# Kernel tuning notes

Hardware: AMD Instinct MI355X
Metric: run time of the kernel (lower is better)

The kernel has to match this reference:

```python
import jax, jax.numpy as jnp
import numpy as np

D_MODEL = 1024
N_HEADS = 16
D_EXP = 4
B, SQ, SKV = 2, 2048, 2048
LN_EPS = 1e-5


def _linear_params(key, d_in, d_out):
    kw, kb = jax.random.split(key)
    w = jax.random.normal(kw, (d_in, d_out), jnp.float32) * 0.02  # stored [in,out]
    b = jax.random.normal(kb, (d_out,), jnp.float32) * 0.02
    return w, b


def setup_inputs() -> dict:
    key = jax.random.key(0)
    ks = jax.random.split(key, 16)
    inp = {}
    inp["x"] = jax.random.normal(ks[0], (B, SQ, D_MODEL), jnp.float32)
    inp["encoder_out"] = jax.random.normal(ks[1], (B, SKV, D_MODEL), jnp.float32)
    # causal target mask, broadcast over batch and heads
    inp["tgt_mask"] = jnp.tril(jnp.ones((SQ, SQ), jnp.int32))[None, None]
    inp["src_mask"] = jnp.ones((1, 1, SQ, SKV), jnp.int32)
    # self-attention params
    inp["wq_s"], inp["bq_s"] = _linear_params(ks[2], D_MODEL, D_MODEL)
    inp["wk_s"], inp["bk_s"] = _linear_params(ks[3], D_MODEL, D_MODEL)
    inp["wv_s"], inp["bv_s"] = _linear_params(ks[4], D_MODEL, D_MODEL)
    inp["wo_s"], inp["bo_s"] = _linear_params(ks[5], D_MODEL, D_MODEL)
    # cross-attention params
    inp["wq_c"], inp["bq_c"] = _linear_params(ks[6], D_MODEL, D_MODEL)
    inp["wk_c"], inp["bk_c"] = _linear_params(ks[7], D_MODEL, D_MODEL)
    inp["wv_c"], inp["bv_c"] = _linear_params(ks[8], D_MODEL, D_MODEL)
    inp["wo_c"], inp["bo_c"] = _linear_params(ks[9], D_MODEL, D_MODEL)
    # feedforward params
    inp["ff1_w"], inp["ff1_b"] = _linear_params(ks[10], D_MODEL, D_MODEL * D_EXP)
    inp["ff2_w"], inp["ff2_b"] = _linear_params(ks[11], D_MODEL * D_EXP, D_MODEL)
    # layernorm params (3 AddNorms)
    for i, k in zip((1, 2, 3), (ks[12], ks[13], ks[14])):
        inp[f"ln{i}_g"] = jnp.ones((D_MODEL,), jnp.float32)
        inp[f"ln{i}_b"] = jnp.zeros((D_MODEL,), jnp.float32)
    return inp


def _layernorm(x, g, b):
    mu = jnp.mean(x, axis=-1, keepdims=True)
    var = jnp.mean(jnp.square(x - mu), axis=-1, keepdims=True)
    return (x - mu) / jnp.sqrt(var + LN_EPS) * g + b


def _mha(xq, xkv, wq, bq, wk, bk, wv, bv, wo, bo, mask):
    Bq, Sq, D = xq.shape
    Hd = D // N_HEADS
    q = (xq @ wq + bq).reshape(Bq, Sq, N_HEADS, Hd).transpose(0, 2, 1, 3)   # bhqd
    k = (xkv @ wk + bk).reshape(Bq, -1, N_HEADS, Hd).transpose(0, 2, 1, 3)  # bhkd
    v = (xkv @ wv + bv).reshape(Bq, -1, N_HEADS, Hd).transpose(0, 2, 1, 3)  # bhkd
    score = jnp.einsum("bhqd,bhkd->bhqk", q, k) / jnp.sqrt(jnp.float32(Hd))
    score = jnp.where(mask == 0, -jnp.inf, score)
    attn = jax.nn.softmax(score, axis=-1)
    ctx = jnp.einsum("bhqk,bhkd->bhqd", attn, v)
    ctx = ctx.transpose(0, 2, 1, 3).reshape(Bq, Sq, D)
    return ctx @ wo + bo


def reference(x, encoder_out, tgt_mask, src_mask,
              wq_s, bq_s, wk_s, bk_s, wv_s, bv_s, wo_s, bo_s,
              wq_c, bq_c, wk_c, bk_c, wv_c, bv_c, wo_c, bo_c,
              ff1_w, ff1_b, ff2_w, ff2_b,
              ln1_g, ln1_b, ln2_g, ln2_b, ln3_g, ln3_b):
    # dropout is identity in eval mode
    sa = _mha(x, x, wq_s, bq_s, wk_s, bk_s, wv_s, bv_s, wo_s, bo_s, tgt_mask)
    h = _layernorm(x + sa, ln1_g, ln1_b)
    ca = _mha(h, encoder_out, wq_c, bq_c, wk_c, bk_c, wv_c, bv_c, wo_c, bo_c, src_mask)
    h2 = _layernorm(h + ca, ln2_g, ln2_b)
    ff = jax.nn.relu(h2 @ ff1_w + ff1_b) @ ff2_w + ff2_b
    return _layernorm(h2 + ff, ln3_g, ln3_b)
```

## Files before the change

kernel.cpp:

```cpp
#include <hip/hip_runtime.h>
#include <stdint.h>

typedef __bf16 bf16;
typedef __attribute__((ext_vector_type(4))) float f32x4;
typedef __attribute__((ext_vector_type(8))) __bf16 bf16x8;
typedef __attribute__((ext_vector_type(4))) __bf16 bf16x4;
typedef __attribute__((ext_vector_type(4))) short s16x4;

#define DM   1024
#define NH   16
#define HDIM 64
#define BB   2
#define SEQ  2048
#define MR   (BB * SEQ)
#define DFF  4096
#define MEG  (1024 * 1024)

__global__ void detect_kernel(const unsigned int* __restrict__ xw,
                              int* __restrict__ flag) {
  int tid = threadIdx.x;
  int bad = 0;
  for (int i = tid; i < 4096; i += 64) {
    unsigned int w = xw[i];
    float flo = __uint_as_float((w & 0xffffu) << 16);
    if (!(fabsf(flo) < 100.f)) bad = 1;
  }
  unsigned long long m = __ballot(bad);
  if (tid == 0) *flag = (m == 0ull) ? 1 : 0;
}

__global__ __launch_bounds__(256) void cvt_big_kernel(
    const void* __restrict__ src, bf16* __restrict__ dst, int n4,
    const int* __restrict__ flag) {
  int i = blockIdx.x * 256 + threadIdx.x;
  if (i >= n4) return;
  if (*flag) {
    ((bf16x4*)dst)[i] = ((const bf16x4*)src)[i];
  } else {
    float4 v = ((const float4*)src)[i];
    bf16x4 o = {(bf16)v.x, (bf16)v.y, (bf16)v.z, (bf16)v.w};
    ((bf16x4*)dst)[i] = o;
  }
}

struct P16 { const void* p[16]; };
__global__ __launch_bounds__(256) void cvt_small_kernel(
    P16 ps, bf16* __restrict__ dstbase, const int* __restrict__ flag) {
  const int ncnt[16] = {1024,1024,1024,1024,1024,1024,1024,1024,
                        4096,1024,1024,1024,1024,1024,1024,1024};
  const int doff[16] = {0,1024,2048,3072,4096,5120,6144,7168,
                        8192,12288,13312,14336,15360,16384,17408,18432};
  int b = blockIdx.x;
  int n = ncnt[b];
  bool isbf = (*flag) != 0;
  const void* s = ps.p[b];
  bf16* d = dstbase + doff[b];
  for (int i = threadIdx.x; i * 4 < n; i += 256) {
    if (isbf) {
      ((bf16x4*)d)[i] = ((const bf16x4*)s)[i];
    } else {
      float4 v = ((const float4*)s)[i];
      bf16x4 o = {(bf16)v.x, (bf16)v.y, (bf16)v.z, (bf16)v.w};
      ((bf16x4*)d)[i] = o;
    }
  }
}

static __device__ __forceinline__ void gl_lds16(const bf16* g, bf16* l) {
  auto gp = reinterpret_cast<__attribute__((address_space(1))) unsigned int*>(
      reinterpret_cast<uintptr_t>(g));
  auto lp = reinterpret_cast<__attribute__((address_space(3))) unsigned int*>(
      (unsigned int)reinterpret_cast<uintptr_t>(l));
  __builtin_amdgcn_global_load_lds(gp, lp, 16, 0, 0);
}

static __device__ __forceinline__ s16x4 as_s16x4(bf16x4 v) {
  s16x4 r;
  __builtin_memcpy(&r, &v, 8);
  return r;
}

struct WTB {
  const void* src[10];
  int dstoff[10];
  int K[10], N[10];
  int bstart[10];
};
__global__ __launch_bounds__(256) void wt_all_kernel(WTB wb, bf16* __restrict__ wtbase,
                                                     const int* __restrict__ flag) {
  __shared__ alignas(16) bf16 tile[64][40];
  int bid = blockIdx.x;
  int wi = 0;
  while (wi < 9 && bid >= wb.bstart[wi + 1]) ++wi;
  int rel = bid - wb.bstart[wi];
  int N = wb.N[wi], K = wb.K[wi];
  int nb = N >> 6;
  int n0 = (rel % nb) * 64, k0 = (rel / nb) * 32;
  const void* w = wb.src[wi];
  bf16* wt = wtbase + wb.dstoff[wi];
  bool isbf = (*flag) != 0;
  int tid = threadIdx.x;
  int np = tid & 31, tk = tid >> 5;
#pragma unroll
  for (int i = 0; i < 4; ++i) {
    int kl = tk + i * 8;
    bf16 b0, b1;
    if (isbf) {
      unsigned int u = *(const unsigned int*)(
          (const bf16*)w + (size_t)(k0 + kl) * N + n0 + np * 2);
      unsigned short s0 = (unsigned short)(u & 0xffffu);
      unsigned short s1 = (unsigned short)(u >> 16);
      __builtin_memcpy(&b0, &s0, 2);
      __builtin_memcpy(&b1, &s1, 2);
    } else {
      const float* fp = (const float*)w + (size_t)(k0 + kl) * N + n0 + np * 2;
      b0 = (bf16)fp[0];
      b1 = (bf16)fp[1];
    }
    tile[np * 2][kl] = b0;
    tile[np * 2 + 1][kl] = b1;
  }
  __syncthreads();
  int nl = tid >> 2, kq = tid & 3;
  bf16x8 v = *(const bf16x8*)(&tile[nl][kq * 8]);
  *(bf16x8*)(wt + (size_t)(n0 + nl) * K + k0 + kq * 8) = v;
}

template <int TM>
__global__ __launch_bounds__(256) void gemm_kernel(
    const bf16* __restrict__ A, const bf16* __restrict__ Bt,
    const bf16* __restrict__ bias, bf16* __restrict__ outb,
    int M, int N, int K, int relu) {
  constexpr int NI = TM / 32;
  constexpr int WM = TM / 2;
  constexpr int CA = TM / 64;
  __shared__ alignas(16) bf16 As[TM * 32];
  __shared__ alignas(16) bf16 Bs[128 * 32];
  int tid = threadIdx.x;
  int lane = tid & 63, wv = tid >> 6;
  int quad = lane >> 4, l15 = lane & 15;
  int m0 = blockIdx.y * TM, n0 = blockIdx.x * 128;
  int wm = wv >> 1, wn = wv & 1;

  f32x4 acc[NI][4];
#pragma unroll
  for (int i = 0; i < NI; ++i)
#pragma unroll
    for (int j = 0; j < 4; ++j) acc[i][j] = (f32x4){0.f, 0.f, 0.f, 0.f};

  int sr = lane >> 2, sc = (lane & 3) * 8;
  const bf16* gA[CA];
  bf16* lA[CA];
#pragma unroll
  for (int t = 0; t < CA; ++t) {
    int ch = wv * CA + t;
    gA[t] = A + (size_t)(m0 + ch * 16 + sr) * K + sc;
    lA[t] = As + ch * 512 + lane * 8;
  }
  const bf16* gB0 = Bt + (size_t)(n0 + (wv * 2) * 16 + sr) * K + sc;
  const bf16* gB1 = Bt + (size_t)(n0 + (wv * 2 + 1) * 16 + sr) * K + sc;
  bf16* lB0 = Bs + (wv * 2) * 512 + lane * 8;
  bf16* lB1 = Bs + (wv * 2 + 1) * 512 + lane * 8;

  for (int k0 = 0; k0 < K; k0 += 32) {
#pragma unroll
    for (int t = 0; t < CA; ++t) gl_lds16(gA[t] + k0, lA[t]);
    gl_lds16(gB0 + k0, lB0);
    gl_lds16(gB1 + k0, lB1);
    __syncthreads();
    bf16x8 af[NI], bfr[4];
#pragma unroll
    for (int i = 0; i < NI; ++i)
      af[i] = *(const bf16x8*)(As + (wm * WM + i * 16 + l15) * 32 + quad * 8);
#pragma unroll
    for (int j = 0; j < 4; ++j)
      bfr[j] = *(const bf16x8*)(Bs + (wn * 64 + j * 16 + l15) * 32 + quad * 8);
#pragma unroll
    for (int i = 0; i < NI; ++i)
#pragma unroll
      for (int j = 0; j < 4; ++j)
        acc[i][j] = __builtin_amdgcn_mfma_f32_16x16x32_bf16(af[i], bfr[j],
                                                            acc[i][j], 0, 0, 0);
    __syncthreads();
  }

#pragma unroll
  for (int j = 0; j < 4; ++j) {
    int col = n0 + wn * 64 + j * 16 + l15;
    float bval = (float)bias[col];
#pragma unroll
    for (int i = 0; i < NI; ++i) {
      int rb = m0 + wm * WM + i * 16 + quad * 4;
#pragma unroll
      for (int r = 0; r < 4; ++r) {
        float v = acc[i][j][r] + bval;
        if (relu) v = fmaxf(v, 0.f);
        outb[(size_t)(rb + r) * N + col] = (bf16)v;
      }
    }
  }
}

__global__ __launch_bounds__(256) void gemm_splitk_kernel(
    const bf16* __restrict__ A, const bf16* __restrict__ Bt,
    float* __restrict__ pout, int M, int N, int KC, int Ktot) {
  __shared__ alignas(16) bf16 As[128 * 32];
  __shared__ alignas(16) bf16 Bs[128 * 32];
  int tid = threadIdx.x;
  int lane = tid & 63, wv = tid >> 6;
  int quad = lane >> 4, l15 = lane & 15;
  int m0 = blockIdx.y * 128, n0 = blockIdx.x * 128;
  int wm = wv >> 1, wn = wv & 1;
  int kb = blockIdx.z * KC;
  pout += (size_t)blockIdx.z * M * N;

  f32x4 acc[4][4];
#pragma unroll
  for (int i = 0; i < 4; ++i)
#pragma unroll
    for (int j = 0; j < 4; ++j) acc[i][j] = (f32x4){0.f, 0.f, 0.f, 0.f};

  int sr = lane >> 2, sc = (lane & 3) * 8;
  const bf16* gA0 = A + (size_t)(m0 + (wv * 2) * 16 + sr) * Ktot + sc;
  const bf16* gA1 = A + (size_t)(m0 + (wv * 2 + 1) * 16 + sr) * Ktot + sc;
  const bf16* gB0 = Bt + (size_t)(n0 + (wv * 2) * 16 + sr) * Ktot + sc;
  const bf16* gB1 = Bt + (size_t)(n0 + (wv * 2 + 1) * 16 + sr) * Ktot + sc;
  bf16* lA0 = As + (wv * 2) * 512 + lane * 8;
  bf16* lA1 = As + (wv * 2 + 1) * 512 + lane * 8;
  bf16* lB0 = Bs + (wv * 2) * 512 + lane * 8;
  bf16* lB1 = Bs + (wv * 2 + 1) * 512 + lane * 8;

  for (int k0 = kb; k0 < kb + KC; k0 += 32) {
    gl_lds16(gA0 + k0, lA0);
    gl_lds16(gA1 + k0, lA1);
    gl_lds16(gB0 + k0, lB0);
    gl_lds16(gB1 + k0, lB1);
    __syncthreads();
    bf16x8 af[4], bfr[4];
#pragma unroll
    for (int i = 0; i < 4; ++i)
      af[i] = *(const bf16x8*)(As + (wm * 64 + i * 16 + l15) * 32 + quad * 8);
#pragma unroll
    for (int j = 0; j < 4; ++j)
      bfr[j] = *(const bf16x8*)(Bs + (wn * 64 + j * 16 + l15) * 32 + quad * 8);
#pragma unroll
    for (int i = 0; i < 4; ++i)
#pragma unroll
      for (int j = 0; j < 4; ++j)
        acc[i][j] = __builtin_amdgcn_mfma_f32_16x16x32_bf16(af[i], bfr[j],
                                                            acc[i][j], 0, 0, 0);
    __syncthreads();
  }
#pragma unroll
  for (int j = 0; j < 4; ++j) {
    int col = n0 + wn * 64 + j * 16 + l15;
#pragma unroll
    for (int i = 0; i < 4; ++i) {
      int rb = m0 + wm * 64 + i * 16 + quad * 4;
#pragma unroll
      for (int r = 0; r < 4; ++r)
        pout[(size_t)(rb + r) * N + col] = acc[i][j][r];
    }
  }
}

__global__ __launch_bounds__(256) void vt_pre_kernel(
    const bf16* __restrict__ v, int vstride, bf16* __restrict__ vt, int skv) {
  __shared__ bf16 tile[32][33];
  int tid = threadIdx.x;
  int tx = tid & 31, ty = tid >> 5;
  int kv0 = blockIdx.x * 32, d0 = blockIdx.y * 32;
  int bh = blockIdx.z;
  int b = bh >> 4, h = bh & 15;
  const bf16* src = v + (size_t)b * skv * vstride + h * HDIM;
#pragma unroll
  for (int i = 0; i < 4; ++i)
    tile[ty + i * 8][tx] = src[(size_t)(kv0 + ty + i * 8) * vstride + d0 + tx];
  __syncthreads();
  bf16* dst = vt + ((size_t)bh * HDIM + d0) * skv + kv0;
#pragma unroll
  for (int i = 0; i < 4; ++i)
    dst[(size_t)(ty + i * 8) * skv + tx] = tile[tx][ty + i * 8];
}

__global__ __launch_bounds__(256, 4) void flash9_kernel(
    const bf16* __restrict__ Q, int qstride,
    const bf16* __restrict__ Kk, int kstride,
    const bf16* __restrict__ VT, bf16* __restrict__ ctx,
    float* __restrict__ opart, float* __restrict__ lpart,
    int skv, int causal, int nsplit) {
  __shared__ alignas(16) bf16 KTl[2][64 * 64];
  __shared__ alignas(16) bf16 VTl[2][64 * 64];
  int tid = threadIdx.x;
  int lane = tid & 63, wv = tid >> 6, quad = lane >> 4, l15 = lane & 15;
  int wg = blockIdx.x;
  int cpx = gridDim.x >> 3;
  int w = (wg & 7) * cpx + (wg >> 3);
  int qb = w & 15;
  int h = (w >> 4) & 15;
  int zz = w >> 8;
  int b = zz / nsplit;
  int half = zz - b * nsplit;
  int q0 = qb * 128;
  int qw = q0 + wv * 32;
  int l7 = l15 & 7;

  bf16x8 qf[2][2];
  const float qsc = 0.125f * 1.44269504f;
#pragma unroll
  for (int a = 0; a < 2; ++a) {
    const bf16* qp = Q + (size_t)(b * SEQ + qw + a * 16 + l15) * qstride + h * HDIM;
    qf[a][0] = *(const bf16x8*)(qp + quad * 8);
    qf[a][1] = *(const bf16x8*)(qp + 32 + quad * 8);
#pragma unroll
    for (int j = 0; j < 8; ++j) {
      qf[a][0][j] = (bf16)((float)qf[a][0][j] * qsc);
      qf[a][1][j] = (bf16)((float)qf[a][1][j] * qsc);
    }
  }
  s16x4 onesA = {0x3F80, 0x3F80, 0x3F80, 0x3F80};

  f32x4 o[2][4], oL[2];
#pragma unroll
  for (int a = 0; a < 2; ++a) {
    oL[a] = (f32x4){0.f, 0.f, 0.f, 0.f};
#pragma unroll
    for (int j = 0; j < 4; ++j) o[a][j] = (f32x4){0.f, 0.f, 0.f, 0.f};
  }

  int nch_tot = causal ? (q0 + 128) / 64 : skv / 64;
  int c_lo = (half * nch_tot) / nsplit;
  int c_hi = ((half + 1) * nch_tot) / nsplit;

  int l8 = lane >> 3;
  int colseg = (lane & 7) ^ l8;
  int grow = wv * 16 + l8;
  const bf16* kbase = Kk + ((size_t)b * skv + grow) * kstride + h * HDIM + colseg * 8;
  const bf16* vbase = VT + ((size_t)(b * NH + h) * HDIM + grow) * skv + colseg * 8;
  bf16* kls = &KTl[0][wv * 1024];
  bf16* vls = &VTl[0][wv * 1024];

  auto STAGE = [&](int bb, int cc) {
    const bf16* ks = kbase + (size_t)(cc * 64) * kstride;
    const bf16* vs = vbase + cc * 64;
    bf16* kd = kls + bb * 4096;
    bf16* vd = vls + bb * 4096;
    gl_lds16(ks, kd);
    gl_lds16(ks + (size_t)8 * kstride, kd + 512);
    gl_lds16(vs, vd);
    gl_lds16(vs + (size_t)8 * skv, vd + 512);
  };

  if (c_lo < c_hi) STAGE(0, c_lo);

  for (int c = c_lo; c < c_hi; ++c) {
    int cur = (c - c_lo) & 1;
    int kv0 = c * 64;
    __syncthreads();
    if (c + 1 < c_hi) STAGE(cur ^ 1, c + 1);

    if (!causal || kv0 <= qw + 31) {
      const bf16* kt_base = &KTl[0][0] + cur * 4096;
      const bf16* vt_base = &VTl[0][0] + cur * 4096;
      bf16x4 p[2][4];
#pragma unroll
      for (int t = 0; t < 4; ++t) {
        const bf16* kb = kt_base + (t * 16 + l15) * 64;
        bf16x8 kt0 = *(const bf16x8*)(kb + ((quad ^ l7) << 3));
        bf16x8 kt1 = *(const bf16x8*)(kb + (((quad + 4) ^ l7) << 3));
#pragma unroll
        for (int a = 0; a < 2; ++a) {
          f32x4 z = (f32x4){0.f, 0.f, 0.f, 0.f};
          z = __builtin_amdgcn_mfma_f32_16x16x32_bf16(kt0, qf[a][0], z, 0, 0, 0);
          z = __builtin_amdgcn_mfma_f32_16x16x32_bf16(kt1, qf[a][1], z, 0, 0, 0);
          if (causal && kv0 + 63 > qw) {
#pragma unroll
            for (int r = 0; r < 4; ++r)
              if (kv0 + t * 16 + quad * 4 + r > qw + a * 16 + l15)
                z[r] = -1e30f;
          }
          bf16x4 pk;
#pragma unroll
          for (int r = 0; r < 4; ++r) pk[r] = (bf16)exp2f(z[r]);
          p[a][t] = pk;
          oL[a] = __builtin_amdgcn_mfma_f32_16x16x16bf16_1k(
              onesA, as_s16x4(pk), oL[a], 0, 0, 0);
        }
      }
#pragma unroll
      for (int jt = 0; jt < 4; ++jt) {
        const bf16* vb = vt_base + (jt * 16 + l15) * 64;
        bf16x4 af[4];
#pragma unroll
        for (int t = 0; t < 4; ++t)
          af[t] = *(const bf16x4*)(
              vb + ((((t * 2 + (quad >> 1)) ^ l7) << 3) + ((quad & 1) << 2)));
#pragma unroll
        for (int a = 0; a < 2; ++a)
#pragma unroll
          for (int t = 0; t < 4; ++t)
            o[a][jt] = __builtin_amdgcn_mfma_f32_16x16x16bf16_1k(
                as_s16x4(af[t]), as_s16x4(p[a][t]), o[a][jt], 0, 0, 0);
      }
    }
  }

  if (nsplit == 1) {
#pragma unroll
    for (int a = 0; a < 2; ++a) {
      float inv = 1.0f / fmaxf(oL[a][0], 1e-30f);
      bf16* cp = ctx + (size_t)(b * SEQ + qw + a * 16 + l15) * DM + h * HDIM + quad * 4;
#pragma unroll
      for (int jt = 0; jt < 4; ++jt) {
        bf16x4 ob = {(bf16)(o[a][jt][0] * inv), (bf16)(o[a][jt][1] * inv),
                     (bf16)(o[a][jt][2] * inv), (bf16)(o[a][jt][3] * inv)};
        *(bf16x4*)(cp + jt * 16) = ob;
      }
    }
  } else {
#pragma unroll
    for (int a = 0; a < 2; ++a) {
      float* op = opart + (size_t)half * MR * DM +
                  (size_t)(b * SEQ + qw + a * 16 + l15) * DM + h * HDIM + quad * 4;
#pragma unroll
      for (int jt = 0; jt < 4; ++jt) *(f32x4*)(op + jt * 16) = o[a][jt];
      if (lane < 16)
        lpart[(size_t)((half * BB + b) * NH + h) * SEQ + qw + a * 16 + l15] =
            oL[a][0];
    }
  }
}

template <int NS>
__global__ __launch_bounds__(256) void flash_comb_kernel(
    const float* __restrict__ opart, const float* __restrict__ lpart,
    bf16* __restrict__ ctx) {
  int row = blockIdx.x, tid = threadIdx.x;
  int b = row >> 11, q = row & (SEQ - 1);
  int h = tid >> 4;
  float l = 0.f;
#pragma unroll
  for (int s = 0; s < NS; ++s)
    l += lpart[(size_t)((s * BB + b) * NH + h) * SEQ + q];
  float inv = 1.0f / fmaxf(l, 1e-30f);
  float a0 = 0.f, a1 = 0.f, a2 = 0.f, a3 = 0.f;
#pragma unroll
  for (int s = 0; s < NS; ++s) {
    f32x4 v = ((const f32x4*)(opart + (size_t)s * MR * DM + (size_t)row * DM))[tid];
    a0 += v[0]; a1 += v[1]; a2 += v[2]; a3 += v[3];
  }
  bf16x4 ob = {(bf16)(a0 * inv), (bf16)(a1 * inv),
               (bf16)(a2 * inv), (bf16)(a3 * inv)};
  ((bf16x4*)(ctx + (size_t)row * DM))[tid] = ob;
}

template <int NP>
__global__ __launch_bounds__(256) void addnorm_red_kernel(
    const bf16* __restrict__ res, const float* __restrict__ part,
    const bf16* __restrict__ bias, const bf16* __restrict__ g,
    const bf16* __restrict__ be, bf16* __restrict__ yb,
    void* __restrict__ outAny, const int* __restrict__ flag) {
  int row = blockIdx.x, tid = threadIdx.x;
  float a0 = 0.f, a1 = 0.f, a2 = 0.f, a3 = 0.f;
#pragma unroll
  for (int p = 0; p < NP; ++p) {
    float4 v = ((const float4*)(part + (size_t)p * MR * DM + (size_t)row * DM))[tid];
    a0 += v.x; a1 += v.y; a2 += v.z; a3 += v.w;
  }
  bf16x4 bb = ((const bf16x4*)bias)[tid];
  bf16x4 rr = ((const bf16x4*)(res + (size_t)row * DM))[tid];
  float s0 = (float)rr[0] + a0 + (float)bb[0];
  float s1 = (float)rr[1] + a1 + (float)bb[1];
  float s2 = (float)rr[2] + a2 + (float)bb[2];
  float s3 = (float)rr[3] + a3 + (float)bb[3];
  float sum = s0 + s1 + s2 + s3;
  float sq = s0 * s0 + s1 * s1 + s2 * s2 + s3 * s3;
#pragma unroll
  for (int mk = 32; mk >= 1; mk >>= 1) {
    sum += __shfl_xor(sum, mk, 64);
    sq += __shfl_xor(sq, mk, 64);
  }
  __shared__ float red[8];
  int wvi = tid >> 6, lane = tid & 63;
  if (lane == 0) { red[wvi * 2] = sum; red[wvi * 2 + 1] = sq; }
  __syncthreads();
  sum = red[0] + red[2] + red[4] + red[6];
  sq = red[1] + red[3] + red[5] + red[7];
  float mu = sum * (1.0f / DM);
  float var = sq * (1.0f / DM) - mu * mu;
  float rstd = rsqrtf(var + 1e-5f);
  bf16x4 g4 = ((const bf16x4*)g)[tid];
  bf16x4 b4 = ((const bf16x4*)be)[tid];
  float y0 = (s0 - mu) * rstd * (float)g4[0] + (float)b4[0];
  float y1 = (s1 - mu) * rstd * (float)g4[1] + (float)b4[1];
  float y2 = (s2 - mu) * rstd * (float)g4[2] + (float)b4[2];
  float y3 = (s3 - mu) * rstd * (float)g4[3] + (float)b4[3];
  if (yb) {
    bf16x4 ob = {(bf16)y0, (bf16)y1, (bf16)y2, (bf16)y3};
    ((bf16x4*)(yb + (size_t)row * DM))[tid] = ob;
  }
  if (outAny) {
    if (*flag) {
      bf16x4 ob = {(bf16)y0, (bf16)y1, (bf16)y2, (bf16)y3};
      ((bf16x4*)outAny)[(size_t)row * 256 + tid] = ob;
    } else {
      ((float4*)outAny)[(size_t)row * 256 + tid] = make_float4(y0, y1, y2, y3);
    }
  }
}

extern "C" void kernel_launch(void* const* d_in, const int* in_sizes, int n_in,
                              void* d_out, int out_size, void* d_ws, size_t ws_size,
                              hipStream_t stream) {
  (void)in_sizes; (void)n_in; (void)out_size; (void)ws_size;
  const void* x_raw   = d_in[0];
  const void* enc_raw = d_in[1];

  char* ws = (char*)d_ws;
  size_t off = 0;
  auto alloc = [&](size_t bytes) -> void* {
    void* p = ws + off;
    off += (bytes + 255) & ~(size_t)255;
    return p;
  };
  const size_t SB = (size_t)MR * DM;
  int* flag    = (int*)alloc(256);
  bf16* smallb = (bf16*)alloc(20480 * 2);
  bf16* wt   = (bf16*)alloc((size_t)16 * MEG * 2);
  bf16* xb   = (bf16*)alloc(SB * 2);
  bf16* encb = (bf16*)alloc(SB * 2);
  bf16* vtg  = (bf16*)alloc(SB * 2);
  bf16* ctx  = (bf16*)alloc(SB * 2);
  bf16* hb1  = (bf16*)alloc(SB * 2);
  bf16* hb2  = (bf16*)alloc(SB * 2);
  bf16* qkv  = (bf16*)alloc(SB * 3 * 2);
  bf16* kvc  = (bf16*)alloc(SB * 2 * 2);
  float* part = (float*)alloc(SB * 4 * 4);
  float* lpart = (float*)alloc((size_t)3 * BB * NH * SEQ * 4);
  bf16* gbuf = qkv;
  bf16* qc   = xb;

  bf16* b_qkvs = smallb + 0;     bf16* b_os  = smallb + 3072;
  bf16* b_qc   = smallb + 4096;  bf16* b_kvc = smallb + 5120;
  bf16* b_oc   = smallb + 7168;  bf16* b_f1  = smallb + 8192;
  bf16* b_f2   = smallb + 12288;
  bf16* l1g = smallb + 13312; bf16* l1b = smallb + 14336;
  bf16* l2g = smallb + 15360; bf16* l2b = smallb + 16384;
  bf16* l3g = smallb + 17408; bf16* l3b = smallb + 18432;

  detect_kernel<<<1, 64, 0, stream>>>((const unsigned int*)x_raw, flag);
  cvt_big_kernel<<<(int)(SB / 1024), 256, 0, stream>>>(x_raw, xb, (int)(SB / 4), flag);
  cvt_big_kernel<<<(int)(SB / 1024), 256, 0, stream>>>(enc_raw, encb, (int)(SB / 4), flag);
  P16 ps;
  ps.p[0] = d_in[5];  ps.p[1] = d_in[7];  ps.p[2] = d_in[9];  ps.p[3] = d_in[11];
  ps.p[4] = d_in[13]; ps.p[5] = d_in[15]; ps.p[6] = d_in[17]; ps.p[7] = d_in[19];
  ps.p[8] = d_in[21]; ps.p[9] = d_in[23];
  ps.p[10] = d_in[24]; ps.p[11] = d_in[25]; ps.p[12] = d_in[26];
  ps.p[13] = d_in[27]; ps.p[14] = d_in[28]; ps.p[15] = d_in[29];
  cvt_small_kernel<<<16, 256, 0, stream>>>(ps, smallb, flag);

  WTB wb;
  const int wsrc[10] = {4, 6, 8, 10, 12, 14, 16, 18, 20, 22};
  for (int i = 0; i < 10; ++i) {
    wb.src[i] = d_in[wsrc[i]];
    wb.K[i] = 1024; wb.N[i] = 1024;
    wb.dstoff[i] = i * MEG;
  }
  wb.N[8] = 4096;
  wb.K[9] = 4096; wb.dstoff[9] = 12 * MEG;
  int bacc = 0;
  for (int i = 0; i < 10; ++i) {
    wb.bstart[i] = bacc;
    bacc += (wb.N[i] / 64) * (wb.K[i] / 32);
  }
  wt_all_kernel<<<bacc, 256, 0, stream>>>(wb, wt, flag);

  gemm_kernel<128><<<dim3(24, 32), 256, 0, stream>>>(xb, wt, b_qkvs, qkv,
                                                     MR, 3072, DM, 0);
  vt_pre_kernel<<<dim3(SEQ / 32, 2, 32), 256, 0, stream>>>(qkv + 2048, 3072, vtg, SEQ);
  flash9_kernel<<<16 * 16 * BB * 2, 256, 0, stream>>>(
      qkv, 3072, qkv + 1024, 3072, vtg, ctx, part, lpart, SEQ, 1, 2);
  flash_comb_kernel<2><<<MR, 256, 0, stream>>>(part, lpart, ctx);
  gemm_splitk_kernel<<<dim3(8, 32, 2), 256, 0, stream>>>(
      ctx, wt + (size_t)3 * MEG, part, MR, DM, 512, DM);
  addnorm_red_kernel<2><<<MR, 256, 0, stream>>>(xb, part, b_os, l1g, l1b,
                                                hb1, nullptr, flag);
  gemm_kernel<64><<<dim3(8, 64), 256, 0, stream>>>(hb1, wt + (size_t)4 * MEG,
                                                   b_qc, qc, MR, DM, DM, 0);
  gemm_kernel<128><<<dim3(16, 32), 256, 0, stream>>>(encb, wt + (size_t)5 * MEG,
                                                     b_kvc, kvc, MR, 2048, DM, 0);
  vt_pre_kernel<<<dim3(SEQ / 32, 2, 32), 256, 0, stream>>>(kvc + 1024, 2048, vtg, SEQ);
  flash9_kernel<<<16 * 16 * BB * 2, 256, 0, stream>>>(
      qc, 1024, kvc, 2048, vtg, ctx, part, lpart, SEQ, 0, 2);
  flash_comb_kernel<2><<<MR, 256, 0, stream>>>(part, lpart, ctx);
  gemm_splitk_kernel<<<dim3(8, 32, 2), 256, 0, stream>>>(
      ctx, wt + (size_t)7 * MEG, part, MR, DM, 512, DM);
  addnorm_red_kernel<2><<<MR, 256, 0, stream>>>(hb1, part, b_oc, l2g, l2b,
                                                hb2, nullptr, flag);
  gemm_kernel<128><<<dim3(32, 32), 256, 0, stream>>>(hb2, wt + (size_t)8 * MEG,
                                                     b_f1, gbuf, MR, DFF, DM, 1);
  gemm_splitk_kernel<<<dim3(8, 32, 4), 256, 0, stream>>>(
      gbuf, wt + (size_t)12 * MEG, part, MR, DM, 1024, DFF);
  addnorm_red_kernel<4><<<MR, 256, 0, stream>>>(hb2, part, b_f2, l3g, l3b,
                                                nullptr, d_out, flag);
}
```

Baseline: 658.0 us.

## Load K tiles straight into registers in flash kernel instead of via LDS

```diff
diff --git a/kernel.cpp b/kernel.cpp
--- a/kernel.cpp
+++ b/kernel.cpp
@@ -283,13 +283,12 @@
     dst[(size_t)(ty + i * 8) * skv + tx] = tile[tx][ty + i * 8];
 }
 
-__global__ __launch_bounds__(256, 4) void flash9_kernel(
+__global__ __launch_bounds__(256, 4) void flash10_kernel(
     const bf16* __restrict__ Q, int qstride,
     const bf16* __restrict__ Kk, int kstride,
     const bf16* __restrict__ VT, bf16* __restrict__ ctx,
     float* __restrict__ opart, float* __restrict__ lpart,
     int skv, int causal, int nsplit) {
-  __shared__ alignas(16) bf16 KTl[2][64 * 64];
   __shared__ alignas(16) bf16 VTl[2][64 * 64];
   int tid = threadIdx.x;
   int lane = tid & 63, wv = tid >> 6, quad = lane >> 4, l15 = lane & 15;
@@ -332,47 +331,50 @@
   int c_lo = (half * nch_tot) / nsplit;
   int c_hi = ((half + 1) * nch_tot) / nsplit;
 
+  const bf16* krow = Kk + ((size_t)b * skv + l15) * kstride + h * HDIM + quad * 8;
+  bf16x8 kt[4][2];
+  auto LOADK = [&](int kv0) {
+#pragma unroll
+    for (int t = 0; t < 4; ++t) {
+      const bf16* p = krow + (size_t)(kv0 + t * 16) * kstride;
+      kt[t][0] = *(const bf16x8*)(p);
+      kt[t][1] = *(const bf16x8*)(p + 32);
+    }
+  };
+
   int l8 = lane >> 3;
   int colseg = (lane & 7) ^ l8;
   int grow = wv * 16 + l8;
-  const bf16* kbase = Kk + ((size_t)b * skv + grow) * kstride + h * HDIM + colseg * 8;
   const bf16* vbase = VT + ((size_t)(b * NH + h) * HDIM + grow) * skv + colseg * 8;
-  bf16* kls = &KTl[0][wv * 1024];
   bf16* vls = &VTl[0][wv * 1024];
-
-  auto STAGE = [&](int bb, int cc) {
-    const bf16* ks = kbase + (size_t)(cc * 64) * kstride;
+  auto STAGEV = [&](int bb, int cc) {
     const bf16* vs = vbase + cc * 64;
-    bf16* kd = kls + bb * 4096;
     bf16* vd = vls + bb * 4096;
-    gl_lds16(ks, kd);
-    gl_lds16(ks + (size_t)8 * kstride, kd + 512);
     gl_lds16(vs, vd);
     gl_lds16(vs + (size_t)8 * skv, vd + 512);
   };
 
-  if (c_lo < c_hi) STAGE(0, c_lo);
+  if (c_lo < c_hi) {
+    STAGEV(0, c_lo);
+    LOADK(c_lo * 64);
+  }
 
   for (int c = c_lo; c < c_hi; ++c) {
     int cur = (c - c_lo) & 1;
     int kv0 = c * 64;
     __syncthreads();
-    if (c + 1 < c_hi) STAGE(cur ^ 1, c + 1);
-
-    if (!causal || kv0 <= qw + 31) {
-      const bf16* kt_base = &KTl[0][0] + cur * 4096;
-      const bf16* vt_base = &VTl[0][0] + cur * 4096;
-      bf16x4 p[2][4];
+    if (c + 1 < c_hi) STAGEV(cur ^ 1, c + 1);
+
+    bool active = !causal || kv0 <= qw + 31;
+    bf16x4 p[2][4];
+    if (active) {
 #pragma unroll
       for (int t = 0; t < 4; ++t) {
-        const bf16* kb = kt_base + (t * 16 + l15) * 64;
-        bf16x8 kt0 = *(const bf16x8*)(kb + ((quad ^ l7) << 3));
-        bf16x8 kt1 = *(const bf16x8*)(kb + (((quad + 4) ^ l7) << 3));
 #pragma unroll
         for (int a = 0; a < 2; ++a) {
           f32x4 z = (f32x4){0.f, 0.f, 0.f, 0.f};
-          z = __builtin_amdgcn_mfma_f32_16x16x32_bf16(kt0, qf[a][0], z, 0, 0, 0);
-          z = __builtin_amdgcn_mfma_f32_16x16x32_bf16(kt1, qf[a][1], z, 0, 0, 0);
+          z = __builtin_amdgcn_mfma_f32_16x16x32_bf16(kt[t][0], qf[a][0], z, 0, 0, 0);
+          z = __builtin_amdgcn_mfma_f32_16x16x32_bf16(kt[t][1], qf[a][1], z, 0, 0, 0);
           if (causal && kv0 + 63 > qw) {
 #pragma unroll
             for (int r = 0; r < 4; ++r)
@@ -387,6 +389,13 @@
               onesA, as_s16x4(pk), oL[a], 0, 0, 0);
         }
       }
+    }
+    if (c + 1 < c_hi) {
+      bool nactive = !causal || (kv0 + 64) <= qw + 31;
+      if (nactive) LOADK(kv0 + 64);
+    }
+    if (active) {
+      const bf16* vt_base = &VTl[0][0] + cur * 4096;
 #pragma unroll
       for (int jt = 0; jt < 4; ++jt) {
         const bf16* vb = vt_base + (jt * 16 + l15) * 64;
@@ -578,7 +587,7 @@
   gemm_kernel<128><<<dim3(24, 32), 256, 0, stream>>>(xb, wt, b_qkvs, qkv,
                                                      MR, 3072, DM, 0);
   vt_pre_kernel<<<dim3(SEQ / 32, 2, 32), 256, 0, stream>>>(qkv + 2048, 3072, vtg, SEQ);
-  flash9_kernel<<<16 * 16 * BB * 2, 256, 0, stream>>>(
+  flash10_kernel<<<16 * 16 * BB * 2, 256, 0, stream>>>(
       qkv, 3072, qkv + 1024, 3072, vtg, ctx, part, lpart, SEQ, 1, 2);
   flash_comb_kernel<2><<<MR, 256, 0, stream>>>(part, lpart, ctx);
   gemm_splitk_kernel<<<dim3(8, 32, 2), 256, 0, stream>>>(
@@ -590,7 +599,7 @@
   gemm_kernel<128><<<dim3(16, 32), 256, 0, stream>>>(encb, wt + (size_t)5 * MEG,
                                                      b_kvc, kvc, MR, 2048, DM, 0);
   vt_pre_kernel<<<dim3(SEQ / 32, 2, 32), 256, 0, stream>>>(kvc + 1024, 2048, vtg, SEQ);
-  flash9_kernel<<<16 * 16 * BB * 2, 256, 0, stream>>>(
+  flash10_kernel<<<16 * 16 * BB * 2, 256, 0, stream>>>(
       qc, 1024, kvc, 2048, vtg, ctx, part, lpart, SEQ, 0, 2);
   flash_comb_kernel<2><<<MR, 256, 0, stream>>>(part, lpart, ctx);
   gemm_splitk_kernel<<<dim3(8, 32, 2), 256, 0, stream>>>(
```

Result: slower. 755.1 us (+14.8%).

## Double K-step per sync in GEMMs and remap workgroups across XCDs

Applied to the files above, without the earlier changes.

```diff
diff --git a/kernel.cpp b/kernel.cpp
--- a/kernel.cpp
+++ b/kernel.cpp
@@ -130,16 +130,19 @@
 __global__ __launch_bounds__(256) void gemm_kernel(
     const bf16* __restrict__ A, const bf16* __restrict__ Bt,
     const bf16* __restrict__ bias, bf16* __restrict__ outb,
-    int M, int N, int K, int relu) {
+    int M, int N, int K, int relu, int nbx) {
   constexpr int NI = TM / 32;
   constexpr int WM = TM / 2;
   constexpr int CA = TM / 64;
-  __shared__ alignas(16) bf16 As[TM * 32];
-  __shared__ alignas(16) bf16 Bs[128 * 32];
+  __shared__ alignas(16) bf16 As[2][TM * 32];
+  __shared__ alignas(16) bf16 Bs[2][128 * 32];
   int tid = threadIdx.x;
   int lane = tid & 63, wv = tid >> 6;
   int quad = lane >> 4, l15 = lane & 15;
-  int m0 = blockIdx.y * TM, n0 = blockIdx.x * 128;
+  int wg = blockIdx.x;
+  int w = (wg & 7) * (gridDim.x >> 3) + (wg >> 3);
+  int bx = w % nbx, by = w / nbx;
+  int m0 = by * TM, n0 = bx * 128;
   int wm = wv >> 1, wn = wv & 1;
 
   f32x4 acc[NI][4];
@@ -150,37 +153,49 @@
 
   int sr = lane >> 2, sc = (lane & 3) * 8;
   const bf16* gA[CA];
-  bf16* lA[CA];
+  bf16* lA0[CA];
+  bf16* lA1[CA];
 #pragma unroll
   for (int t = 0; t < CA; ++t) {
     int ch = wv * CA + t;
     gA[t] = A + (size_t)(m0 + ch * 16 + sr) * K + sc;
-    lA[t] = As + ch * 512 + lane * 8;
+    lA0[t] = As[0] + ch * 512 + lane * 8;
+    lA1[t] = As[1] + ch * 512 + lane * 8;
   }
   const bf16* gB0 = Bt + (size_t)(n0 + (wv * 2) * 16 + sr) * K + sc;
   const bf16* gB1 = Bt + (size_t)(n0 + (wv * 2 + 1) * 16 + sr) * K + sc;
-  bf16* lB0 = Bs + (wv * 2) * 512 + lane * 8;
-  bf16* lB1 = Bs + (wv * 2 + 1) * 512 + lane * 8;
-
-  for (int k0 = 0; k0 < K; k0 += 32) {
-#pragma unroll
-    for (int t = 0; t < CA; ++t) gl_lds16(gA[t] + k0, lA[t]);
-    gl_lds16(gB0 + k0, lB0);
-    gl_lds16(gB1 + k0, lB1);
+  bf16* lB00 = Bs[0] + (wv * 2) * 512 + lane * 8;
+  bf16* lB01 = Bs[1] + (wv * 2) * 512 + lane * 8;
+  bf16* lB10 = Bs[0] + (wv * 2 + 1) * 512 + lane * 8;
+  bf16* lB11 = Bs[1] + (wv * 2 + 1) * 512 + lane * 8;
+
+  for (int k0 = 0; k0 < K; k0 += 64) {
+#pragma unroll
+    for (int t = 0; t < CA; ++t) {
+      gl_lds16(gA[t] + k0, lA0[t]);
+      gl_lds16(gA[t] + k0 + 32, lA1[t]);
+    }
+    gl_lds16(gB0 + k0, lB00);
+    gl_lds16(gB0 + k0 + 32, lB01);
+    gl_lds16(gB1 + k0, lB10);
+    gl_lds16(gB1 + k0 + 32, lB11);
     __syncthreads();
-    bf16x8 af[NI], bfr[4];
-#pragma unroll
-    for (int i = 0; i < NI; ++i)
-      af[i] = *(const bf16x8*)(As + (wm * WM + i * 16 + l15) * 32 + quad * 8);
-#pragma unroll
-    for (int j = 0; j < 4; ++j)
-      bfr[j] = *(const bf16x8*)(Bs + (wn * 64 + j * 16 + l15) * 32 + quad * 8);
-#pragma unroll
-    for (int i = 0; i < NI; ++i)
+#pragma unroll
+    for (int s = 0; s < 2; ++s) {
+      bf16x8 af[NI], bfr[4];
+#pragma unroll
+      for (int i = 0; i < NI; ++i)
+        af[i] = *(const bf16x8*)(As[s] + (wm * WM + i * 16 + l15) * 32 + quad * 8);
 #pragma unroll
       for (int j = 0; j < 4; ++j)
-        acc[i][j] = __builtin_amdgcn_mfma_f32_16x16x32_bf16(af[i], bfr[j],
-                                                            acc[i][j], 0, 0, 0);
+        bfr[j] = *(const bf16x8*)(Bs[s] + (wn * 64 + j * 16 + l15) * 32 + quad * 8);
+#pragma unroll
+      for (int i = 0; i < NI; ++i)
+#pragma unroll
+        for (int j = 0; j < 4; ++j)
+          acc[i][j] = __builtin_amdgcn_mfma_f32_16x16x32_bf16(af[i], bfr[j],
+                                                              acc[i][j], 0, 0, 0);
+    }
     __syncthreads();
   }
 
@@ -203,16 +218,22 @@
 
 __global__ __launch_bounds__(256) void gemm_splitk_kernel(
     const bf16* __restrict__ A, const bf16* __restrict__ Bt,
-    float* __restrict__ pout, int M, int N, int KC, int Ktot) {
-  __shared__ alignas(16) bf16 As[128 * 32];
-  __shared__ alignas(16) bf16 Bs[128 * 32];
+    float* __restrict__ pout, int M, int N, int KC, int Ktot, int nbx) {
+  __shared__ alignas(16) bf16 As[2][128 * 32];
+  __shared__ alignas(16) bf16 Bs[2][128 * 32];
   int tid = threadIdx.x;
   int lane = tid & 63, wv = tid >> 6;
   int quad = lane >> 4, l15 = lane & 15;
-  int m0 = blockIdx.y * 128, n0 = blockIdx.x * 128;
+  int wg = blockIdx.x;
+  int w = (wg & 7) * (gridDim.x >> 3) + (wg >> 3);
+  int nxy = nbx * (M >> 7);
+  int bz = w / nxy;
+  int rem = w - bz * nxy;
+  int bx = rem % nbx, by = rem / nbx;
+  int m0 = by * 128, n0 = bx * 128;
   int wm = wv >> 1, wn = wv & 1;
-  int kb = blockIdx.z * KC;
-  pout += (size_t)blockIdx.z * M * N;
+  int kb = bz * KC;
+  pout += (size_t)bz * M * N;
 
   f32x4 acc[4][4];
 #pragma unroll
@@ -225,30 +246,41 @@
   const bf16* gA1 = A + (size_t)(m0 + (wv * 2 + 1) * 16 + sr) * Ktot + sc;
   const bf16* gB0 = Bt + (size_t)(n0 + (wv * 2) * 16 + sr) * Ktot + sc;
   const bf16* gB1 = Bt + (size_t)(n0 + (wv * 2 + 1) * 16 + sr) * Ktot + sc;
-  bf16* lA0 = As + (wv * 2) * 512 + lane * 8;
-  bf16* lA1 = As + (wv * 2 + 1) * 512 + lane * 8;
-  bf16* lB0 = Bs + (wv * 2) * 512 + lane * 8;
-  bf16* lB1 = Bs + (wv * 2 + 1) * 512 + lane * 8;
-
-  for (int k0 = kb; k0 < kb + KC; k0 += 32) {
-    gl_lds16(gA0 + k0, lA0);
-    gl_lds16(gA1 + k0, lA1);
-    gl_lds16(gB0 + k0, lB0);
-    gl_lds16(gB1 + k0, lB1);
+  bf16* lA00 = As[0] + (wv * 2) * 512 + lane * 8;
+  bf16* lA01 = As[1] + (wv * 2) * 512 + lane * 8;
+  bf16* lA10 = As[0] + (wv * 2 + 1) * 512 + lane * 8;
+  bf16* lA11 = As[1] + (wv * 2 + 1) * 512 + lane * 8;
+  bf16* lB00 = Bs[0] + (wv * 2) * 512 + lane * 8;
+  bf16* lB01 = Bs[1] + (wv * 2) * 512 + lane * 8;
+  bf16* lB10 = Bs[0] + (wv * 2 + 1) * 512 + lane * 8;
+  bf16* lB11 = Bs[1] + (wv * 2 + 1) * 512 + lane * 8;
+
+  for (int k0 = kb; k0 < kb + KC; k0 += 64) {
+    gl_lds16(gA0 + k0, lA00);
+    gl_lds16(gA0 + k0 + 32, lA01);
+    gl_lds16(gA1 + k0, lA10);
+    gl_lds16(gA1 + k0 + 32, lA11);
+    gl_lds16(gB0 + k0, lB00);
+    gl_lds16(gB0 + k0 + 32, lB01);
+    gl_lds16(gB1 + k0, lB10);
+    gl_lds16(gB1 + k0 + 32, lB11);
     __syncthreads();
-    bf16x8 af[4], bfr[4];
-#pragma unroll
-    for (int i = 0; i < 4; ++i)
-      af[i] = *(const bf16x8*)(As + (wm * 64 + i * 16 + l15) * 32 + quad * 8);
-#pragma unroll
-    for (int j = 0; j < 4; ++j)
-      bfr[j] = *(const bf16x8*)(Bs + (wn * 64 + j * 16 + l15) * 32 + quad * 8);
-#pragma unroll
-    for (int i = 0; i < 4; ++i)
+#pragma unroll
+    for (int s = 0; s < 2; ++s) {
+      bf16x8 af[4], bfr[4];
+#pragma unroll
+      for (int i = 0; i < 4; ++i)
+        af[i] = *(const bf16x8*)(As[s] + (wm * 64 + i * 16 + l15) * 32 + quad * 8);
 #pragma unroll
       for (int j = 0; j < 4; ++j)
-        acc[i][j] = __builtin_amdgcn_mfma_f32_16x16x32_bf16(af[i], bfr[j],
-                                                            acc[i][j], 0, 0, 0);
+        bfr[j] = *(const bf16x8*)(Bs[s] + (wn * 64 + j * 16 + l15) * 32 + quad * 8);
+#pragma unroll
+      for (int i = 0; i < 4; ++i)
+#pragma unroll
+        for (int j = 0; j < 4; ++j)
+          acc[i][j] = __builtin_amdgcn_mfma_f32_16x16x32_bf16(af[i], bfr[j],
+                                                              acc[i][j], 0, 0, 0);
+    }
     __syncthreads();
   }
 #pragma unroll
@@ -575,32 +607,32 @@
   }
   wt_all_kernel<<<bacc, 256, 0, stream>>>(wb, wt, flag);
 
-  gemm_kernel<128><<<dim3(24, 32), 256, 0, stream>>>(xb, wt, b_qkvs, qkv,
-                                                     MR, 3072, DM, 0);
+  gemm_kernel<128><<<24 * 32, 256, 0, stream>>>(xb, wt, b_qkvs, qkv,
+                                                MR, 3072, DM, 0, 24);
   vt_pre_kernel<<<dim3(SEQ / 32, 2, 32), 256, 0, stream>>>(qkv + 2048, 3072, vtg, SEQ);
   flash9_kernel<<<16 * 16 * BB * 2, 256, 0, stream>>>(
       qkv, 3072, qkv + 1024, 3072, vtg, ctx, part, lpart, SEQ, 1, 2);
   flash_comb_kernel<2><<<MR, 256, 0, stream>>>(part, lpart, ctx);
-  gemm_splitk_kernel<<<dim3(8, 32, 2), 256, 0, stream>>>(
-      ctx, wt + (size_t)3 * MEG, part, MR, DM, 512, DM);
+  gemm_splitk_kernel<<<8 * 32 * 2, 256, 0, stream>>>(
+      ctx, wt + (size_t)3 * MEG, part, MR, DM, 512, DM, 8);
   addnorm_red_kernel<2><<<MR, 256, 0, stream>>>(xb, part, b_os, l1g, l1b,
                                                 hb1, nullptr, flag);
-  gemm_kernel<64><<<dim3(8, 64), 256, 0, stream>>>(hb1, wt + (size_t)4 * MEG,
-                                                   b_qc, qc, MR, DM, DM, 0);
-  gemm_kernel<128><<<dim3(16, 32), 256, 0, stream>>>(encb, wt + (size_t)5 * MEG,
-                                                     b_kvc, kvc, MR, 2048, DM, 0);
+  gemm_kernel<64><<<8 * 64, 256, 0, stream>>>(hb1, wt + (size_t)4 * MEG,
+                                              b_qc, qc, MR, DM, DM, 0, 8);
+  gemm_kernel<128><<<16 * 32, 256, 0, stream>>>(encb, wt + (size_t)5 * MEG,
+                                                b_kvc, kvc, MR, 2048, DM, 0, 16);
   vt_pre_kernel<<<dim3(SEQ / 32, 2, 32), 256, 0, stream>>>(kvc + 1024, 2048, vtg, SEQ);
   flash9_kernel<<<16 * 16 * BB * 2, 256, 0, stream>>>(
       qc, 1024, kvc, 2048, vtg, ctx, part, lpart, SEQ, 0, 2);
   flash_comb_kernel<2><<<MR, 256, 0, stream>>>(part, lpart, ctx);
-  gemm_splitk_kernel<<<dim3(8, 32, 2), 256, 0, stream>>>(
-      ctx, wt + (size_t)7 * MEG, part, MR, DM, 512, DM);
+  gemm_splitk_kernel<<<8 * 32 * 2, 256, 0, stream>>>(
+      ctx, wt + (size_t)7 * MEG, part, MR, DM, 512, DM, 8);
   addnorm_red_kernel<2><<<MR, 256, 0, stream>>>(hb1, part, b_oc, l2g, l2b,
                                                 hb2, nullptr, flag);
-  gemm_kernel<128><<<dim3(32, 32), 256, 0, stream>>>(hb2, wt + (size_t)8 * MEG,
-                                                     b_f1, gbuf, MR, DFF, DM, 1);
-  gemm_splitk_kernel<<<dim3(8, 32, 4), 256, 0, stream>>>(
-      gbuf, wt + (size_t)12 * MEG, part, MR, DM, 1024, DFF);
+  gemm_kernel<128><<<32 * 32, 256, 0, stream>>>(hb2, wt + (size_t)8 * MEG,
+                                                b_f1, gbuf, MR, DFF, DM, 1, 32);
+  gemm_splitk_kernel<<<8 * 32 * 4, 256, 0, stream>>>(
+      gbuf, wt + (size_t)12 * MEG, part, MR, DM, 1024, DFF, 8);
   addnorm_red_kernel<4><<<MR, 256, 0, stream>>>(hb2, part, b_f2, l3g, l3b,
                                                 nullptr, d_out, flag);
 }
```

New measurement: 636.0 us. -3.3%, faster.
